# Performance work log

Measured on AMD Instinct MI355X. Metric: run time of the kernel, lower is better.

Reference implementation:

```python
import jax, jax.numpy as jnp
import numpy as np

N = 100000      # nodes
E = 1600000     # edges (avg degree 16)
F_IN = 128      # node feature dim
F_E = 8         # edge feature dim
H = 4           # attention heads (layer 1)
C = 16          # hidden per head
T = 1           # target size (layer 2, heads=1, concat=False)
NEG_SLOPE = 0.2


def setup_inputs() -> dict:
    key = jax.random.key(0)
    ks = jax.random.split(key, 20)
    g = lambda k, shape, fan: (jax.random.normal(k, shape, jnp.float32) / np.sqrt(fan))
    return {
        "x": jax.random.normal(ks[0], (N, F_IN), jnp.float32),
        "edge_index": jax.random.randint(ks[1], (2, E), 0, N, dtype=jnp.int32),
        "edge_attr": jax.random.normal(ks[2], (E, F_E), jnp.float32),
        # layer 1 (in=F_IN, out=C, heads=H, concat=True, edge_dim=F_E)
        "Wl1": g(ks[3], (F_IN, H * C), F_IN),
        "bl1": jnp.zeros((H * C,), jnp.float32),
        "Wr1": g(ks[4], (F_IN, H * C), F_IN),
        "br1": jnp.zeros((H * C,), jnp.float32),
        "We1": g(ks[5], (F_E, H * C), F_E),
        "att1": g(ks[6], (H, C), C),
        "b1": jnp.zeros((H * C,), jnp.float32),
        # layer 2 (in=H*C, out=T, heads=1, concat=False, edge_dim=F_E)
        "Wl2": g(ks[7], (H * C, T), H * C),
        "bl2": jnp.zeros((T,), jnp.float32),
        "Wr2": g(ks[8], (H * C, T), H * C),
        "br2": jnp.zeros((T,), jnp.float32),
        "We2": g(ks[9], (F_E, T), F_E),
        "att2": g(ks[10], (1, T), T),
        "b2": jnp.zeros((T,), jnp.float32),
    }


def _gatv2(x, src, dst, eattr, Wl, bl, Wr, br, We, att, bias, heads, out_ch, concat, n_nodes):
    # add self loops, self-loop edge_attr = mean of edge_attr (PyG fill_value='mean')
    loop = jnp.arange(n_nodes, dtype=src.dtype)
    src_a = jnp.concatenate([src, loop])
    dst_a = jnp.concatenate([dst, loop])
    ea = jnp.concatenate(
        [eattr, jnp.broadcast_to(eattr.mean(axis=0), (n_nodes, eattr.shape[1]))], axis=0)

    xl = (x @ Wl + bl).reshape(n_nodes, heads, out_ch)   # source transform
    xr = (x @ Wr + br).reshape(n_nodes, heads, out_ch)   # target transform
    ee = (ea @ We).reshape(-1, heads, out_ch)            # edge transform (no bias)

    # GATv2: score = att . LeakyReLU(x_l[src] + x_r[dst] + W_e e)
    s = jax.nn.leaky_relu(xl[src_a] + xr[dst_a] + ee, NEG_SLOPE)  # [Ea,H,C]
    logits = jnp.einsum('ehc,hc->eh', s, att)                      # [Ea,H]

    # segment softmax over destination nodes (every node has a self loop)
    m = jax.ops.segment_max(logits, dst_a, num_segments=n_nodes)   # [N,H]
    p = jnp.exp(logits - m[dst_a])
    denom = jax.ops.segment_sum(p, dst_a, num_segments=n_nodes)
    alpha = p / denom[dst_a]                                        # [Ea,H]

    out = jax.ops.segment_sum(xl[src_a] * alpha[:, :, None], dst_a,
                              num_segments=n_nodes)                 # [N,H,C]
    out = out.reshape(n_nodes, heads * out_ch) if concat else out.mean(axis=1)
    return out + bias


def reference(x, edge_index, edge_attr, Wl1, bl1, Wr1, br1, We1, att1, b1,
              Wl2, bl2, Wr2, br2, We2, att2, b2):
    src, dst = edge_index[0], edge_index[1]
    # dropout layers are identity at eval time (training=False)
    h = _gatv2(x, src, dst, edge_attr, Wl1, bl1, Wr1, br1, We1, att1, b1,
               H, C, True, N)
    h = jax.nn.elu(h)
    out = _gatv2(h, src, dst, edge_attr, Wl2, bl2, Wr2, br2, We2, att2, b2,
                 1, T, False, N)
    return out
```

## Files before the change

kernel.cpp:

```cpp
#include <hip/hip_runtime.h>
#include <hip/hip_fp16.h>
#include <math.h>

#define N_NODES 100000
#define N_EDGES 1600000
#define N_ITEMS (N_EDGES + N_NODES)
#define F_IN 128
#define F_E 8
#define HC 64
#define NHEAD 4
#define NEG 0.2f
#define SCAN_BS 1024
#define SCAN_NB ((N_NODES + SCAN_BS - 1) / SCAN_BS)
#define MS_BLOCKS 1024
#define NEG_BIG (-3.0e38f)

union H2I { __half2 h; int i; };

__global__ void mean_sum_kernel(const float* __restrict__ ea, float* __restrict__ partials,
                                unsigned* __restrict__ deg) {
    __shared__ float sh[4][8];
    int stride = gridDim.x * blockDim.x;
    for (int i = blockIdx.x * blockDim.x + threadIdx.x; i < N_NODES; i += stride)
        deg[i] = 1u;
    float acc[8] = {0.f,0.f,0.f,0.f,0.f,0.f,0.f,0.f};
    for (int r = blockIdx.x * blockDim.x + threadIdx.x; r < N_EDGES; r += stride) {
        const float4* p = (const float4*)(ea + (size_t)r * 8);
        float4 a = p[0], b = p[1];
        acc[0] += a.x; acc[1] += a.y; acc[2] += a.z; acc[3] += a.w;
        acc[4] += b.x; acc[5] += b.y; acc[6] += b.z; acc[7] += b.w;
    }
    int wid  = threadIdx.x >> 6;
    int lane = threadIdx.x & 63;
#pragma unroll
    for (int k = 0; k < 8; k++) {
        float v = acc[k];
        for (int off = 32; off; off >>= 1) v += __shfl_down(v, off);
        if (lane == 0) sh[wid][k] = v;
    }
    __syncthreads();
    if (threadIdx.x < 8) {
        float s = sh[0][threadIdx.x] + sh[1][threadIdx.x] + sh[2][threadIdx.x] + sh[3][threadIdx.x];
        partials[blockIdx.x * 8 + threadIdx.x] = s;
    }
}

__global__ void reduce_sum8(const float* __restrict__ partials, float* __restrict__ sum8) {
    int lane = threadIdx.x;
    int c = lane & 7, g = lane >> 3;
    float s = 0.f;
    for (int b = g; b < MS_BLOCKS; b += 8) s += partials[b * 8 + c];
    s += __shfl_xor(s, 8);
    s += __shfl_xor(s, 16);
    s += __shfl_xor(s, 32);
    if (lane < 8) sum8[lane] = s;
}

__global__ void hist_kernel(const int* __restrict__ dst, unsigned* __restrict__ deg) {
    int e = blockIdx.x * blockDim.x + threadIdx.x;
    if (e < N_EDGES) atomicAdd(&deg[dst[e]], 1u);
}

__global__ void scan1(const unsigned* __restrict__ deg, unsigned* __restrict__ local_inc,
                      unsigned* __restrict__ bsum) {
    __shared__ unsigned wsum[16];
    int i = blockIdx.x * SCAN_BS + threadIdx.x;
    int lane = threadIdx.x & 63;
    int wid  = threadIdx.x >> 6;
    unsigned v = (i < N_NODES) ? deg[i] : 0u;
    unsigned sc = v;
#pragma unroll
    for (int off = 1; off < 64; off <<= 1) {
        unsigned t = __shfl_up(sc, off);
        if (lane >= off) sc += t;
    }
    if (lane == 63) wsum[wid] = sc;
    __syncthreads();
    if (threadIdx.x < 16) {
        unsigned w = wsum[threadIdx.x];
#pragma unroll
        for (int off = 1; off < 16; off <<= 1) {
            unsigned t = __shfl_up(w, off);
            if ((int)threadIdx.x >= off) w += t;
        }
        wsum[threadIdx.x] = w;
    }
    __syncthreads();
    unsigned base = wid ? wsum[wid - 1] : 0u;
    sc += base;
    if (i < N_NODES) local_inc[i] = sc;
    if (threadIdx.x == SCAN_BS - 1) bsum[blockIdx.x] = sc;
}

__global__ void scan2(unsigned* __restrict__ bsum) {
    __shared__ unsigned tmp[128];
    int t = threadIdx.x;
    unsigned v = (t < SCAN_NB) ? bsum[t] : 0u;
    tmp[t] = v;
    __syncthreads();
    for (int off = 1; off < 128; off <<= 1) {
        unsigned add = (t >= off) ? tmp[t - off] : 0u;
        __syncthreads();
        tmp[t] += add;
        __syncthreads();
    }
    if (t < SCAN_NB) bsum[t] = tmp[t] - v;
}

__global__ void scan3(const unsigned* __restrict__ local_inc, const unsigned* __restrict__ deg,
                      const unsigned* __restrict__ bsum,
                      unsigned* __restrict__ row_start, unsigned* __restrict__ next) {
    int i = blockIdx.x * blockDim.x + threadIdx.x;
    if (i >= N_NODES) return;
    unsigned v = local_inc[i] - deg[i] + bsum[i / SCAN_BS];
    row_start[i] = v;
    next[i] = v;
}

__global__ void scatter_kernel(const int* __restrict__ src, const int* __restrict__ dst,
                               const float* __restrict__ ea, const float* __restrict__ sum8,
                               const float* __restrict__ We2,
                               unsigned* __restrict__ next,
                               int* __restrict__ sorted_src, __half* __restrict__ seah,
                               float* __restrict__ see2) {
    int item = blockIdx.x * blockDim.x + threadIdx.x;
    if (item >= N_ITEMS) return;
    int s, d;
    float4 a, b;
    if (item < N_EDGES) {
        s = src[item]; d = dst[item];
        const float4* p = (const float4*)(ea + (size_t)item * 8);
        a = p[0]; b = p[1];
    } else {
        s = d = item - N_EDGES;
        const float inv = 1.0f / N_EDGES;
        a = make_float4(sum8[0]*inv, sum8[1]*inv, sum8[2]*inv, sum8[3]*inv);
        b = make_float4(sum8[4]*inv, sum8[5]*inv, sum8[6]*inv, sum8[7]*inv);
    }
    float ee2 = a.x*We2[0] + a.y*We2[1] + a.z*We2[2] + a.w*We2[3]
              + b.x*We2[4] + b.y*We2[5] + b.z*We2[6] + b.w*We2[7];
    unsigned pos = atomicAdd(&next[d], 1u);
    sorted_src[pos] = s;
    see2[pos] = ee2;
    H2I p0, p1, p2, p3;
    p0.h = __floats2half2_rn(a.x, a.y);
    p1.h = __floats2half2_rn(a.z, a.w);
    p2.h = __floats2half2_rn(b.x, b.y);
    p3.h = __floats2half2_rn(b.z, b.w);
    *(int4*)(seah + (size_t)pos * 8) = make_int4(p0.i, p1.i, p2.i, p3.i);
}

__global__ __launch_bounds__(256) void gemm1_kernel(
        const float* __restrict__ x,
        const float* __restrict__ Wl, const float* __restrict__ bl,
        const float* __restrict__ Wr, const float* __restrict__ br,
        __half* __restrict__ xlh, float* __restrict__ xr) {
    __shared__ float xs_t[F_IN][36];
    int t = threadIdx.x & 31;
    int g = threadIdx.x >> 5;
    const float* Wsel = (t < 16) ? Wl : Wr;
    const float* bsel = (t < 16) ? bl : br;
    int jc = (t < 16) ? 4 * t : 4 * t - HC;
    float4 bias = *(const float4*)(bsel + jc);

    int n0 = blockIdx.x * 32;
    int row = threadIdx.x >> 3;
    int cq  = threadIdx.x & 7;
#pragma unroll
    for (int r = 0; r < 4; r++) {
        int c = cq * 4 + r * 32;
        float4 v = *(const float4*)(x + (size_t)(n0 + row) * F_IN + c);
        xs_t[c + 0][row] = v.x;
        xs_t[c + 1][row] = v.y;
        xs_t[c + 2][row] = v.z;
        xs_t[c + 3][row] = v.w;
    }
    __syncthreads();
    int nb = g * 4;
    float4 a0 = bias, a1 = bias, a2 = bias, a3 = bias;
#pragma unroll 4
    for (int k = 0; k < F_IN; k++) {
        float4 w  = *(const float4*)(Wsel + k * HC + jc);
        float4 xv = *(const float4*)&xs_t[k][nb];
        a0.x += w.x * xv.x; a0.y += w.y * xv.x; a0.z += w.z * xv.x; a0.w += w.w * xv.x;
        a1.x += w.x * xv.y; a1.y += w.y * xv.y; a1.z += w.z * xv.y; a1.w += w.w * xv.y;
        a2.x += w.x * xv.z; a2.y += w.y * xv.z; a2.z += w.z * xv.z; a2.w += w.w * xv.z;
        a3.x += w.x * xv.w; a3.y += w.y * xv.w; a3.z += w.z * xv.w; a3.w += w.w * xv.w;
    }
    if (t < 16) {
        float4 arr[4] = {a0, a1, a2, a3};
#pragma unroll
        for (int r = 0; r < 4; r++) {
            H2I u0, u1;
            u0.h = __floats2half2_rn(arr[r].x, arr[r].y);
            u1.h = __floats2half2_rn(arr[r].z, arr[r].w);
            *(int2*)(xlh + (size_t)(n0 + nb + r) * HC + jc) = make_int2(u0.i, u1.i);
        }
    } else {
        *(float4*)(xr + (size_t)(n0 + nb + 0) * HC + jc) = a0;
        *(float4*)(xr + (size_t)(n0 + nb + 1) * HC + jc) = a1;
        *(float4*)(xr + (size_t)(n0 + nb + 2) * HC + jc) = a2;
        *(float4*)(xr + (size_t)(n0 + nb + 3) * HC + jc) = a3;
    }
}

__device__ __forceinline__ float4 sea_lo(const int4& r) {
    H2I h0, h1; h0.i = r.x; h1.i = r.y;
    float2 f0 = __half22float2(h0.h), f1 = __half22float2(h1.h);
    return make_float4(f0.x, f0.y, f1.x, f1.y);
}
__device__ __forceinline__ float4 sea_hi(const int4& r) {
    H2I h2, h3; h2.i = r.z; h3.i = r.w;
    float2 f2 = __half22float2(h2.h), f3 = __half22float2(h3.h);
    return make_float4(f2.x, f2.y, f3.x, f3.y);
}
__device__ __forceinline__ float4 xl_f(const int2& w) {
    H2I u0, u1; u0.i = w.x; u1.i = w.y;
    float2 g0 = __half22float2(u0.h), g1 = __half22float2(u1.h);
    return make_float4(g0.x, g0.y, g1.x, g1.y);
}

__device__ __forceinline__ void edge_update(const float4* __restrict__ we,
                                            const float4& attv, const float4& xrv,
                                            bool valid, const float4& ea0, const float4& ea1,
                                            const float4& xlv,
                                            float& m, float& den, float4& acc) {
    float4 v;
    v.x = xlv.x + xrv.x + ea0.x*we[0].x + ea0.y*we[1].x + ea0.z*we[2].x + ea0.w*we[3].x
                        + ea1.x*we[4].x + ea1.y*we[5].x + ea1.z*we[6].x + ea1.w*we[7].x;
    v.y = xlv.y + xrv.y + ea0.x*we[0].y + ea0.y*we[1].y + ea0.z*we[2].y + ea0.w*we[3].y
                        + ea1.x*we[4].y + ea1.y*we[5].y + ea1.z*we[6].y + ea1.w*we[7].y;
    v.z = xlv.z + xrv.z + ea0.x*we[0].z + ea0.y*we[1].z + ea0.z*we[2].z + ea0.w*we[3].z
                        + ea1.x*we[4].z + ea1.y*we[5].z + ea1.z*we[6].z + ea1.w*we[7].z;
    v.w = xlv.w + xrv.w + ea0.x*we[0].w + ea0.y*we[1].w + ea0.z*we[2].w + ea0.w*we[3].w
                        + ea1.x*we[4].w + ea1.y*we[5].w + ea1.z*we[6].w + ea1.w*we[7].w;
    v.x = v.x > 0.f ? v.x : NEG * v.x;
    v.y = v.y > 0.f ? v.y : NEG * v.y;
    v.z = v.z > 0.f ? v.z : NEG * v.z;
    v.w = v.w > 0.f ? v.w : NEG * v.w;
    float prod = v.x*attv.x + v.y*attv.y + v.z*attv.z + v.w*attv.w;
    prod += __shfl_xor(prod, 1);
    prod += __shfl_xor(prod, 2);
    float logit = valid ? prod : NEG_BIG;
    float mnew  = fmaxf(m, logit);
    float scale = __expf(m - mnew);
    float p     = valid ? __expf(logit - mnew) : 0.f;
    den   = den   * scale + p;
    acc.x = acc.x * scale + p * xlv.x;
    acc.y = acc.y * scale + p * xlv.y;
    acc.z = acc.z * scale + p * xlv.z;
    acc.w = acc.w * scale + p * xlv.w;
    m = mnew;
}

__global__ void gat1_kernel(const unsigned* __restrict__ row_start, const unsigned* __restrict__ deg,
                            const int* __restrict__ ssrc, const __half* __restrict__ seah,
                            const float* __restrict__ We1, const float* __restrict__ att1,
                            const float* __restrict__ b1,
                            const __half* __restrict__ xlh, const float* __restrict__ xr,
                            const float* __restrict__ Wl2, const float* __restrict__ bl2,
                            const float* __restrict__ Wr2, const float* __restrict__ br2,
                            float* __restrict__ xl2, float* __restrict__ xr2) {
    int node = blockIdx.x * (blockDim.x >> 6) + (threadIdx.x >> 6);
    int lane = threadIdx.x & 63;
    if (node >= N_NODES) return;
    int g  = lane >> 4;
    int cl = lane & 15;
    unsigned start = row_start[node];
    unsigned cnt   = deg[node];

    int s_reg = ssrc[start + min((unsigned)lane, cnt - 1)];

    float4 we[8];
#pragma unroll
    for (int k = 0; k < 8; k++) we[k] = *(const float4*)(We1 + k * HC + 4 * cl);
    float4 attv = *(const float4*)(att1 + 4 * cl);
    float4 xrv  = *(const float4*)(xr + (size_t)node * HC + 4 * cl);

    float mA = NEG_BIG, denA = 0.f, mB = NEG_BIG, denB = 0.f;
    float4 accA = make_float4(0.f,0.f,0.f,0.f), accB = make_float4(0.f,0.f,0.f,0.f);

    int4 spA0, spA1, spB0, spB1;
    int2 xpA0, xpA1, xpB0, xpB1;

#define ISSUE(S, JJ) do {                                                      \
    unsigned iA_ = min((JJ) + (unsigned)g, cnt - 1);                           \
    unsigned iB_ = min((JJ) + 4u + (unsigned)g, cnt - 1);                      \
    int sA_ = (iA_ < 64u) ? __shfl(s_reg, (int)iA_) : ssrc[start + iA_];       \
    int sB_ = (iB_ < 64u) ? __shfl(s_reg, (int)iB_) : ssrc[start + iB_];       \
    spA##S = *(const int4*)(seah + (size_t)(start + iA_) * 8);                 \
    xpA##S = *(const int2*)(xlh + (size_t)sA_ * HC + 4 * cl);                  \
    spB##S = *(const int4*)(seah + (size_t)(start + iB_) * 8);                 \
    xpB##S = *(const int2*)(xlh + (size_t)sB_ * HC + 4 * cl);                  \
} while (0)

    ISSUE(0, 0u);
    ISSUE(1, 8u);
    for (unsigned j = 0; j < cnt; j += 16) {
        {
            float4 e0A = sea_lo(spA0), e1A = sea_hi(spA0), xA = xl_f(xpA0);
            float4 e0B = sea_lo(spB0), e1B = sea_hi(spB0), xB = xl_f(xpB0);
            if (j + 16 < cnt) ISSUE(0, j + 16);
            edge_update(we, attv, xrv, (j + g) < cnt,      e0A, e1A, xA, mA, denA, accA);
            edge_update(we, attv, xrv, (j + 4 + g) < cnt,  e0B, e1B, xB, mB, denB, accB);
        }
        if (j + 8 < cnt) {
            float4 e0A = sea_lo(spA1), e1A = sea_hi(spA1), xA = xl_f(xpA1);
            float4 e0B = sea_lo(spB1), e1B = sea_hi(spB1), xB = xl_f(xpB1);
            if (j + 24 < cnt) ISSUE(1, j + 24);
            edge_update(we, attv, xrv, (j + 8 + g) < cnt,  e0A, e1A, xA, mA, denA, accA);
            edge_update(we, attv, xrv, (j + 12 + g) < cnt, e0B, e1B, xB, mB, denB, accB);
        }
    }
#undef ISSUE

    float m = fmaxf(mA, mB);
    float sA = __expf(mA - m), sB = __expf(mB - m);
    float den = denA * sA + denB * sB;
    float4 acc;
    acc.x = accA.x * sA + accB.x * sB;
    acc.y = accA.y * sA + accB.y * sB;
    acc.z = accA.z * sA + accB.z * sB;
    acc.w = accA.w * sA + accB.w * sB;

    float M = m;
    M = fmaxf(M, __shfl_xor(M, 16));
    M = fmaxf(M, __shfl_xor(M, 32));
    float gs = __expf(m - M);
    den *= gs; acc.x *= gs; acc.y *= gs; acc.z *= gs; acc.w *= gs;
    den   += __shfl_xor(den, 16);   den   += __shfl_xor(den, 32);
    acc.x += __shfl_xor(acc.x, 16); acc.x += __shfl_xor(acc.x, 32);
    acc.y += __shfl_xor(acc.y, 16); acc.y += __shfl_xor(acc.y, 32);
    acc.z += __shfl_xor(acc.z, 16); acc.z += __shfl_xor(acc.z, 32);
    acc.w += __shfl_xor(acc.w, 16); acc.w += __shfl_xor(acc.w, 32);

    float4 b1v  = *(const float4*)(b1 + 4 * cl);
    float4 wl2v = *(const float4*)(Wl2 + 4 * cl);
    float4 wr2v = *(const float4*)(Wr2 + 4 * cl);
    float inv_den = 1.f / den;
    float4 o;
    o.x = acc.x * inv_den + b1v.x;
    o.y = acc.y * inv_den + b1v.y;
    o.z = acc.z * inv_den + b1v.z;
    o.w = acc.w * inv_den + b1v.w;
    o.x = o.x > 0.f ? o.x : expm1f(o.x);
    o.y = o.y > 0.f ? o.y : expm1f(o.y);
    o.z = o.z > 0.f ? o.z : expm1f(o.z);
    o.w = o.w > 0.f ? o.w : expm1f(o.w);
    float sl = o.x*wl2v.x + o.y*wl2v.y + o.z*wl2v.z + o.w*wl2v.w;
    float sr = o.x*wr2v.x + o.y*wr2v.y + o.z*wr2v.z + o.w*wr2v.w;
#pragma unroll
    for (int off = 1; off <= 8; off <<= 1) {
        sl += __shfl_xor(sl, off);
        sr += __shfl_xor(sr, off);
    }
    if (lane == 0) {
        xl2[node] = sl + bl2[0];
        xr2[node] = sr + br2[0];
    }
}

__global__ void gat2_kernel(const unsigned* __restrict__ row_start, const unsigned* __restrict__ deg,
                            const int* __restrict__ sorted_src, const float* __restrict__ see2,
                            const float* __restrict__ att2,
                            const float* __restrict__ xl2, const float* __restrict__ xr2,
                            const float* __restrict__ b2, float* __restrict__ out) {
    int node = blockIdx.x * (blockDim.x >> 6) + (threadIdx.x >> 6);
    int lane = threadIdx.x & 63;
    if (node >= N_NODES) return;
    unsigned start = row_start[node];
    unsigned cnt   = deg[node];
    float xrv = xr2[node];
    float a2  = att2[0];
    float m = -INFINITY, den = 0.f, num = 0.f;
    for (unsigned base = 0; base < cnt; base += 64) {
        unsigned idx = base + lane;
        float logit = -INFINITY, xv = 0.f;
        if (idx < cnt) {
            int s = sorted_src[start + idx];
            float ee = see2[start + idx];
            xv = xl2[s];
            float v = xv + xrv + ee;
            v = v > 0.f ? v : NEG * v;
            logit = a2 * v;
        }
        float mm = logit;
        for (int off = 1; off < 64; off <<= 1) mm = fmaxf(mm, __shfl_xor(mm, off));
        float mnew = fmaxf(m, mm);
        float p  = (idx < cnt) ? __expf(logit - mnew) : 0.f;
        float pn = p * xv;
        for (int off = 1; off < 64; off <<= 1) {
            p  += __shfl_xor(p, off);
            pn += __shfl_xor(pn, off);
        }
        float scale = __expf(m - mnew);
        den = den * scale + p;
        num = num * scale + pn;
        m = mnew;
    }
    if (lane == 0) out[node] = num / den + b2[0];
}

extern "C" void kernel_launch(void* const* d_in, const int* in_sizes, int n_in,
                              void* d_out, int out_size, void* d_ws, size_t ws_size,
                              hipStream_t stream) {
    const float* x    = (const float*)d_in[0];
    const int*   ei   = (const int*)d_in[1];
    const float* ea   = (const float*)d_in[2];
    const float* Wl1  = (const float*)d_in[3];
    const float* bl1  = (const float*)d_in[4];
    const float* Wr1  = (const float*)d_in[5];
    const float* br1  = (const float*)d_in[6];
    const float* We1  = (const float*)d_in[7];
    const float* att1 = (const float*)d_in[8];
    const float* b1   = (const float*)d_in[9];
    const float* Wl2  = (const float*)d_in[10];
    const float* bl2  = (const float*)d_in[11];
    const float* Wr2  = (const float*)d_in[12];
    const float* br2  = (const float*)d_in[13];
    const float* We2  = (const float*)d_in[14];
    const float* att2 = (const float*)d_in[15];
    const float* b2   = (const float*)d_in[16];

    const int* src = ei;
    const int* dst = ei + N_EDGES;

    float* W = (float*)d_ws;
    size_t o = 0;
    float*    sum8      = W + o;               o += 8;
    float*    partials  = W + o;               o += MS_BLOCKS * 8;
    unsigned* deg       = (unsigned*)(W + o);  o += N_NODES;
    unsigned* local_inc = (unsigned*)(W + o);  o += N_NODES;
    unsigned* bsum      = (unsigned*)(W + o);  o += 128;
    unsigned* row_start = (unsigned*)(W + o);  o += N_NODES;
    unsigned* next      = (unsigned*)(W + o);  o += N_NODES;
    int*      ssrc      = (int*)(W + o);       o += N_ITEMS;
    float*    see2      = W + o;               o += N_ITEMS;
    o = (o + 3) & ~(size_t)3;
    __half*   seah      = (__half*)(W + o);    o += (size_t)N_ITEMS * 4;
    __half*   xl1h      = (__half*)(W + o);    o += (size_t)N_NODES * (HC / 2);
    float*    xr1       = W + o;               o += (size_t)N_NODES * HC;
    float*    xl2       = W + o;               o += N_NODES;
    float*    xr2       = W + o;               o += N_NODES;

    mean_sum_kernel<<<MS_BLOCKS, 256, 0, stream>>>(ea, partials, deg);
    reduce_sum8<<<1, 64, 0, stream>>>(partials, sum8);
    hist_kernel<<<(N_EDGES + 255) / 256, 256, 0, stream>>>(dst, deg);
    scan1<<<SCAN_NB, SCAN_BS, 0, stream>>>(deg, local_inc, bsum);
    scan2<<<1, 128, 0, stream>>>(bsum);
    scan3<<<(N_NODES + 255) / 256, 256, 0, stream>>>(local_inc, deg, bsum, row_start, next);
    scatter_kernel<<<(N_ITEMS + 255) / 256, 256, 0, stream>>>(
        src, dst, ea, sum8, We2, next, ssrc, seah, see2);
    gemm1_kernel<<<N_NODES / 32, 256, 0, stream>>>(x, Wl1, bl1, Wr1, br1, xl1h, xr1);
    gat1_kernel<<<(N_NODES + 3) / 4, 256, 0, stream>>>(
        row_start, deg, ssrc, seah, We1, att1, b1, xl1h, xr1,
        Wl2, bl2, Wr2, br2, xl2, xr2);
    gat2_kernel<<<(N_NODES + 3) / 4, 256, 0, stream>>>(
        row_start, deg, ssrc, see2, att2, xl2, xr2, b2, (float*)d_out);
}
```

Baseline: 439.2 us.

## Make GAT aggregation kernels persistent grid-stride with lighter single-stage prefetch

```diff
diff --git a/kernel.cpp b/kernel.cpp
--- a/kernel.cpp
+++ b/kernel.cpp
@@ -234,10 +234,10 @@
                         + ea1.x*we[4].z + ea1.y*we[5].z + ea1.z*we[6].z + ea1.w*we[7].z;
     v.w = xlv.w + xrv.w + ea0.x*we[0].w + ea0.y*we[1].w + ea0.z*we[2].w + ea0.w*we[3].w
                         + ea1.x*we[4].w + ea1.y*we[5].w + ea1.z*we[6].w + ea1.w*we[7].w;
-    v.x = v.x > 0.f ? v.x : NEG * v.x;
-    v.y = v.y > 0.f ? v.y : NEG * v.y;
-    v.z = v.z > 0.f ? v.z : NEG * v.z;
-    v.w = v.w > 0.f ? v.w : NEG * v.w;
+    v.x = fmaxf(v.x, NEG * v.x);
+    v.y = fmaxf(v.y, NEG * v.y);
+    v.z = fmaxf(v.z, NEG * v.z);
+    v.w = fmaxf(v.w, NEG * v.w);
     float prod = v.x*attv.x + v.y*attv.y + v.z*attv.z + v.w*attv.w;
     prod += __shfl_xor(prod, 1);
     prod += __shfl_xor(prod, 2);
@@ -253,7 +253,9 @@
     m = mnew;
 }
 
-__global__ void gat1_kernel(const unsigned* __restrict__ row_start, const unsigned* __restrict__ deg,
+#define GAT1_BLOCKS 2048
+__global__ __launch_bounds__(256) void gat1_kernel(
+                            const unsigned* __restrict__ row_start, const unsigned* __restrict__ deg,
                             const int* __restrict__ ssrc, const __half* __restrict__ seah,
                             const float* __restrict__ We1, const float* __restrict__ att1,
                             const float* __restrict__ b1,
@@ -261,144 +263,147 @@
                             const float* __restrict__ Wl2, const float* __restrict__ bl2,
                             const float* __restrict__ Wr2, const float* __restrict__ br2,
                             float* __restrict__ xl2, float* __restrict__ xr2) {
-    int node = blockIdx.x * (blockDim.x >> 6) + (threadIdx.x >> 6);
+    int wave  = blockIdx.x * (blockDim.x >> 6) + (threadIdx.x >> 6);
+    int nwave = GAT1_BLOCKS * 4;
     int lane = threadIdx.x & 63;
-    if (node >= N_NODES) return;
     int g  = lane >> 4;
     int cl = lane & 15;
-    unsigned start = row_start[node];
-    unsigned cnt   = deg[node];
-
-    int s_reg = ssrc[start + min((unsigned)lane, cnt - 1)];
 
     float4 we[8];
 #pragma unroll
     for (int k = 0; k < 8; k++) we[k] = *(const float4*)(We1 + k * HC + 4 * cl);
     float4 attv = *(const float4*)(att1 + 4 * cl);
-    float4 xrv  = *(const float4*)(xr + (size_t)node * HC + 4 * cl);
-
-    float mA = NEG_BIG, denA = 0.f, mB = NEG_BIG, denB = 0.f;
-    float4 accA = make_float4(0.f,0.f,0.f,0.f), accB = make_float4(0.f,0.f,0.f,0.f);
-
-    int4 spA0, spA1, spB0, spB1;
-    int2 xpA0, xpA1, xpB0, xpB1;
-
-#define ISSUE(S, JJ) do {                                                      \
-    unsigned iA_ = min((JJ) + (unsigned)g, cnt - 1);                           \
-    unsigned iB_ = min((JJ) + 4u + (unsigned)g, cnt - 1);                      \
-    int sA_ = (iA_ < 64u) ? __shfl(s_reg, (int)iA_) : ssrc[start + iA_];       \
-    int sB_ = (iB_ < 64u) ? __shfl(s_reg, (int)iB_) : ssrc[start + iB_];       \
-    spA##S = *(const int4*)(seah + (size_t)(start + iA_) * 8);                 \
-    xpA##S = *(const int2*)(xlh + (size_t)sA_ * HC + 4 * cl);                  \
-    spB##S = *(const int4*)(seah + (size_t)(start + iB_) * 8);                 \
-    xpB##S = *(const int2*)(xlh + (size_t)sB_ * HC + 4 * cl);                  \
-} while (0)
-
-    ISSUE(0, 0u);
-    ISSUE(1, 8u);
-    for (unsigned j = 0; j < cnt; j += 16) {
-        {
-            float4 e0A = sea_lo(spA0), e1A = sea_hi(spA0), xA = xl_f(xpA0);
-            float4 e0B = sea_lo(spB0), e1B = sea_hi(spB0), xB = xl_f(xpB0);
-            if (j + 16 < cnt) ISSUE(0, j + 16);
-            edge_update(we, attv, xrv, (j + g) < cnt,      e0A, e1A, xA, mA, denA, accA);
-            edge_update(we, attv, xrv, (j + 4 + g) < cnt,  e0B, e1B, xB, mB, denB, accB);
-        }
-        if (j + 8 < cnt) {
-            float4 e0A = sea_lo(spA1), e1A = sea_hi(spA1), xA = xl_f(xpA1);
-            float4 e0B = sea_lo(spB1), e1B = sea_hi(spB1), xB = xl_f(xpB1);
-            if (j + 24 < cnt) ISSUE(1, j + 24);
-            edge_update(we, attv, xrv, (j + 8 + g) < cnt,  e0A, e1A, xA, mA, denA, accA);
-            edge_update(we, attv, xrv, (j + 12 + g) < cnt, e0B, e1B, xB, mB, denB, accB);
-        }
-    }
-#undef ISSUE
-
-    float m = fmaxf(mA, mB);
-    float sA = __expf(mA - m), sB = __expf(mB - m);
-    float den = denA * sA + denB * sB;
-    float4 acc;
-    acc.x = accA.x * sA + accB.x * sB;
-    acc.y = accA.y * sA + accB.y * sB;
-    acc.z = accA.z * sA + accB.z * sB;
-    acc.w = accA.w * sA + accB.w * sB;
-
-    float M = m;
-    M = fmaxf(M, __shfl_xor(M, 16));
-    M = fmaxf(M, __shfl_xor(M, 32));
-    float gs = __expf(m - M);
-    den *= gs; acc.x *= gs; acc.y *= gs; acc.z *= gs; acc.w *= gs;
-    den   += __shfl_xor(den, 16);   den   += __shfl_xor(den, 32);
-    acc.x += __shfl_xor(acc.x, 16); acc.x += __shfl_xor(acc.x, 32);
-    acc.y += __shfl_xor(acc.y, 16); acc.y += __shfl_xor(acc.y, 32);
-    acc.z += __shfl_xor(acc.z, 16); acc.z += __shfl_xor(acc.z, 32);
-    acc.w += __shfl_xor(acc.w, 16); acc.w += __shfl_xor(acc.w, 32);
-
     float4 b1v  = *(const float4*)(b1 + 4 * cl);
     float4 wl2v = *(const float4*)(Wl2 + 4 * cl);
     float4 wr2v = *(const float4*)(Wr2 + 4 * cl);
-    float inv_den = 1.f / den;
-    float4 o;
-    o.x = acc.x * inv_den + b1v.x;
-    o.y = acc.y * inv_den + b1v.y;
-    o.z = acc.z * inv_den + b1v.z;
-    o.w = acc.w * inv_den + b1v.w;
-    o.x = o.x > 0.f ? o.x : expm1f(o.x);
-    o.y = o.y > 0.f ? o.y : expm1f(o.y);
-    o.z = o.z > 0.f ? o.z : expm1f(o.z);
-    o.w = o.w > 0.f ? o.w : expm1f(o.w);
-    float sl = o.x*wl2v.x + o.y*wl2v.y + o.z*wl2v.z + o.w*wl2v.w;
-    float sr = o.x*wr2v.x + o.y*wr2v.y + o.z*wr2v.z + o.w*wr2v.w;
-#pragma unroll
-    for (int off = 1; off <= 8; off <<= 1) {
-        sl += __shfl_xor(sl, off);
-        sr += __shfl_xor(sr, off);
-    }
-    if (lane == 0) {
-        xl2[node] = sl + bl2[0];
-        xr2[node] = sr + br2[0];
-    }
-}
-
-__global__ void gat2_kernel(const unsigned* __restrict__ row_start, const unsigned* __restrict__ deg,
+    float bl2s = bl2[0], br2s = br2[0];
+
+    for (int node = wave; node < N_NODES; node += nwave) {
+        unsigned start = row_start[node];
+        unsigned cnt   = deg[node];
+        unsigned cm1   = cnt - 1;
+        float4 xrv = *(const float4*)(xr + (size_t)node * HC + 4 * cl);
+
+        float mA = NEG_BIG, denA = 0.f, mB = NEG_BIG, denB = 0.f;
+        float4 accA = make_float4(0.f,0.f,0.f,0.f), accB = make_float4(0.f,0.f,0.f,0.f);
+
+#define IDXA(J) (start + min((J) + (unsigned)g, cm1))
+#define IDXB(J) (start + min((J) + 4u + (unsigned)g, cm1))
+        int sA = ssrc[IDXA(0u)], sB = ssrc[IDXB(0u)];
+        int4 spA = *(const int4*)(seah + (size_t)IDXA(0u) * 8);
+        int4 spB = *(const int4*)(seah + (size_t)IDXB(0u) * 8);
+        int2 xpA = *(const int2*)(xlh + (size_t)sA * HC + 4 * cl);
+        int2 xpB = *(const int2*)(xlh + (size_t)sB * HC + 4 * cl);
+        int sA_n = ssrc[IDXA(8u)], sB_n = ssrc[IDXB(8u)];
+
+        for (unsigned j = 0; j < cnt; j += 8) {
+            float4 e0A = sea_lo(spA), e1A = sea_hi(spA), xA = xl_f(xpA);
+            float4 e0B = sea_lo(spB), e1B = sea_hi(spB), xB = xl_f(xpB);
+            bool vA = (j + g) < cnt, vB = (j + 4 + g) < cnt;
+            if (j + 8 < cnt) {
+                spA = *(const int4*)(seah + (size_t)IDXA(j + 8) * 8);
+                spB = *(const int4*)(seah + (size_t)IDXB(j + 8) * 8);
+                xpA = *(const int2*)(xlh + (size_t)sA_n * HC + 4 * cl);
+                xpB = *(const int2*)(xlh + (size_t)sB_n * HC + 4 * cl);
+                if (j + 16 < cnt) {
+                    sA_n = ssrc[IDXA(j + 16)];
+                    sB_n = ssrc[IDXB(j + 16)];
+                }
+            }
+            edge_update(we, attv, xrv, vA, e0A, e1A, xA, mA, denA, accA);
+            edge_update(we, attv, xrv, vB, e0B, e1B, xB, mB, denB, accB);
+        }
+#undef IDXA
+#undef IDXB
+
+        float m = fmaxf(mA, mB);
+        float sAc = __expf(mA - m), sBc = __expf(mB - m);
+        float den = denA * sAc + denB * sBc;
+        float4 acc;
+        acc.x = accA.x * sAc + accB.x * sBc;
+        acc.y = accA.y * sAc + accB.y * sBc;
+        acc.z = accA.z * sAc + accB.z * sBc;
+        acc.w = accA.w * sAc + accB.w * sBc;
+
+        float M = m;
+        M = fmaxf(M, __shfl_xor(M, 16));
+        M = fmaxf(M, __shfl_xor(M, 32));
+        float gs = __expf(m - M);
+        den *= gs; acc.x *= gs; acc.y *= gs; acc.z *= gs; acc.w *= gs;
+        den   += __shfl_xor(den, 16);   den   += __shfl_xor(den, 32);
+        acc.x += __shfl_xor(acc.x, 16); acc.x += __shfl_xor(acc.x, 32);
+        acc.y += __shfl_xor(acc.y, 16); acc.y += __shfl_xor(acc.y, 32);
+        acc.z += __shfl_xor(acc.z, 16); acc.z += __shfl_xor(acc.z, 32);
+        acc.w += __shfl_xor(acc.w, 16); acc.w += __shfl_xor(acc.w, 32);
+
+        float inv_den = 1.f / den;
+        float4 o;
+        o.x = acc.x * inv_den + b1v.x;
+        o.y = acc.y * inv_den + b1v.y;
+        o.z = acc.z * inv_den + b1v.z;
+        o.w = acc.w * inv_den + b1v.w;
+        o.x = o.x > 0.f ? o.x : __expf(o.x) - 1.f;
+        o.y = o.y > 0.f ? o.y : __expf(o.y) - 1.f;
+        o.z = o.z > 0.f ? o.z : __expf(o.z) - 1.f;
+        o.w = o.w > 0.f ? o.w : __expf(o.w) - 1.f;
+        float sl = o.x*wl2v.x + o.y*wl2v.y + o.z*wl2v.z + o.w*wl2v.w;
+        float sr = o.x*wr2v.x + o.y*wr2v.y + o.z*wr2v.z + o.w*wr2v.w;
+#pragma unroll
+        for (int off = 1; off <= 8; off <<= 1) {
+            sl += __shfl_xor(sl, off);
+            sr += __shfl_xor(sr, off);
+        }
+        if (lane == 0) {
+            xl2[node] = sl + bl2s;
+            xr2[node] = sr + br2s;
+        }
+    }
+}
+
+#define GAT2_BLOCKS 2048
+__global__ __launch_bounds__(256) void gat2_kernel(
+                            const unsigned* __restrict__ row_start, const unsigned* __restrict__ deg,
                             const int* __restrict__ sorted_src, const float* __restrict__ see2,
                             const float* __restrict__ att2,
                             const float* __restrict__ xl2, const float* __restrict__ xr2,
                             const float* __restrict__ b2, float* __restrict__ out) {
-    int node = blockIdx.x * (blockDim.x >> 6) + (threadIdx.x >> 6);
+    int wave  = blockIdx.x * (blockDim.x >> 6) + (threadIdx.x >> 6);
+    int nwave = GAT2_BLOCKS * 4;
     int lane = threadIdx.x & 63;
-    if (node >= N_NODES) return;
-    unsigned start = row_start[node];
-    unsigned cnt   = deg[node];
-    float xrv = xr2[node];
-    float a2  = att2[0];
-    float m = -INFINITY, den = 0.f, num = 0.f;
-    for (unsigned base = 0; base < cnt; base += 64) {
-        unsigned idx = base + lane;
-        float logit = -INFINITY, xv = 0.f;
-        if (idx < cnt) {
-            int s = sorted_src[start + idx];
-            float ee = see2[start + idx];
-            xv = xl2[s];
-            float v = xv + xrv + ee;
-            v = v > 0.f ? v : NEG * v;
-            logit = a2 * v;
-        }
-        float mm = logit;
-        for (int off = 1; off < 64; off <<= 1) mm = fmaxf(mm, __shfl_xor(mm, off));
-        float mnew = fmaxf(m, mm);
-        float p  = (idx < cnt) ? __expf(logit - mnew) : 0.f;
-        float pn = p * xv;
-        for (int off = 1; off < 64; off <<= 1) {
-            p  += __shfl_xor(p, off);
-            pn += __shfl_xor(pn, off);
-        }
-        float scale = __expf(m - mnew);
-        den = den * scale + p;
-        num = num * scale + pn;
-        m = mnew;
-    }
-    if (lane == 0) out[node] = num / den + b2[0];
+    float a2 = att2[0];
+    float b2s = b2[0];
+    for (int node = wave; node < N_NODES; node += nwave) {
+        unsigned start = row_start[node];
+        unsigned cnt   = deg[node];
+        float xrv = xr2[node];
+        float m = -INFINITY, den = 0.f, num = 0.f;
+        for (unsigned base = 0; base < cnt; base += 64) {
+            unsigned idx = base + lane;
+            float logit = -INFINITY, xv = 0.f;
+            if (idx < cnt) {
+                int s = sorted_src[start + idx];
+                float ee = see2[start + idx];
+                xv = xl2[s];
+                float v = xv + xrv + ee;
+                v = fmaxf(v, NEG * v);
+                logit = a2 * v;
+            }
+            float mm = logit;
+            for (int off = 1; off < 64; off <<= 1) mm = fmaxf(mm, __shfl_xor(mm, off));
+            float mnew = fmaxf(m, mm);
+            float p  = (idx < cnt) ? __expf(logit - mnew) : 0.f;
+            float pn = p * xv;
+            for (int off = 1; off < 64; off <<= 1) {
+                p  += __shfl_xor(p, off);
+                pn += __shfl_xor(pn, off);
+            }
+            float scale = __expf(m - mnew);
+            den = den * scale + p;
+            num = num * scale + pn;
+            m = mnew;
+        }
+        if (lane == 0) out[node] = num / den + b2s;
+    }
 }
 
 extern "C" void kernel_launch(void* const* d_in, const int* in_sizes, int n_in,
@@ -452,9 +457,9 @@
     scatter_kernel<<<(N_ITEMS + 255) / 256, 256, 0, stream>>>(
         src, dst, ea, sum8, We2, next, ssrc, seah, see2);
     gemm1_kernel<<<N_NODES / 32, 256, 0, stream>>>(x, Wl1, bl1, Wr1, br1, xl1h, xr1);
-    gat1_kernel<<<(N_NODES + 3) / 4, 256, 0, stream>>>(
+    gat1_kernel<<<GAT1_BLOCKS, 256, 0, stream>>>(
         row_start, deg, ssrc, seah, We1, att1, b1, xl1h, xr1,
         Wl2, bl2, Wr2, br2, xl2, xr2);
-    gat2_kernel<<<(N_NODES + 3) / 4, 256, 0, stream>>>(
+    gat2_kernel<<<GAT2_BLOCKS, 256, 0, stream>>>(
         row_start, deg, ssrc, see2, att2, xl2, xr2, b2, (float*)d_out);
 }
```

Result: slower. 452.3 us (+3.0%).
